# Kernel optimization log

Hardware: AMD Instinct MI355X
Metric: run time of the kernel (lower is better)

Reference implementation:

```python
import jax, jax.numpy as jnp
import numpy as np
from jax import lax

D_MODEL = 1024
STATE_DIM = 32
GROUPS = 8
GROUP_DIM = D_MODEL // GROUPS
DT_MIN = 0.001
DT_MAX = 0.1
EPS = 1e-6


def setup_inputs() -> dict:
    key = jax.random.key(0)
    ks = jax.random.split(key, 6)
    B, T = 4, 4096
    u = jax.random.normal(ks[0], (B, T, D_MODEL), dtype=jnp.float32)
    state = jnp.zeros((B, GROUPS, STATE_DIM), dtype=jnp.float32)
    A_log = jax.random.normal(ks[1], (GROUPS, STATE_DIM), dtype=jnp.float32) * 0.02
    B_param = jax.random.normal(ks[2], (GROUPS, STATE_DIM, GROUP_DIM), dtype=jnp.float32) * 0.02
    C = jax.random.normal(ks[3], (GROUPS, GROUP_DIM, STATE_DIM), dtype=jnp.float32) * 0.02
    Dp = jnp.zeros((GROUPS, GROUP_DIM), dtype=jnp.float32)
    dt_logit = jnp.zeros((GROUPS,), dtype=jnp.float32)
    return {"u": u, "state": state, "A_log": A_log, "B_param": B_param,
            "C": C, "Dp": Dp, "dt_logit": dt_logit}


def reference(u, state, A_log, B_param, C, Dp, dt_logit):
    Bsz, T, Dm = u.shape
    A = -jax.nn.softplus(A_log)                                  # [G,N]
    dt = DT_MIN + (DT_MAX - DT_MIN) * jax.nn.sigmoid(dt_logit)   # [G]
    dt_g = dt[:, None]                                           # [G,1]
    Abar = jnp.exp(A * dt_g)                                     # [G,N]
    # (exp(A dt) - 1)/A, stable for small |A|
    frac = jnp.where(jnp.abs(A) > EPS, (Abar - 1.0) / A,
                     jnp.broadcast_to(dt_g, A.shape))            # [G,N]
    Bbar = frac[..., None] * B_param                             # [G,N,gd]

    u_g = u.reshape(Bsz, T, GROUPS, GROUP_DIM)                   # [B,T,G,gd]
    # precompute input injections for all timesteps, then scan the LTI recurrence
    Bu = jnp.einsum('btgi,gni->btgn', u_g, Bbar)                 # [B,T,G,N]
    Bu_t = jnp.moveaxis(Bu, 1, 0)                                # [T,B,G,N]

    def step(s, bu):
        s = s * Abar + bu                                        # [B,G,N]
        return s, s

    s_final, states = lax.scan(step, state, Bu_t)                # states: [T,B,G,N]
    Cs = jnp.einsum('tbgn,gdn->btgd', states, C)                 # [B,T,G,gd]
    y = (Cs + Dp * u_g).reshape(Bsz, T, Dm)                      # [B,T,D]
    return y, s_final
```

## Files before the change

kernel.cpp:

```cpp
#include <hip/hip_runtime.h>
#include <hip/hip_bf16.h>

#define DM 1024
#define SD 32
#define NG 8
#define GD 128
#define BS 4
#define TT 4096
#define CL 64
#define NC (TT/CL)

typedef __attribute__((ext_vector_type(8))) short short8;
typedef __attribute__((ext_vector_type(4))) float f32x4;

#define WS_POWA  0
#define WS_STL   65536
#define WS_CARRY (WS_STL + 8388608)
#define WS_PAL   (WS_CARRY + 262144)

__device__ __forceinline__ unsigned short f2bf(float f) {
  __hip_bfloat16 h = __float2bfloat16(f);
  return __builtin_bit_cast(unsigned short, h);
}
__device__ __forceinline__ float bf2f(unsigned short h) {
  return __uint_as_float(((unsigned)h) << 16);
}
__device__ __forceinline__ float softplus_f(float x) {
  return (x > 20.f) ? x : log1pf(expf(x));
}
__device__ __forceinline__ short8 pack8(float4 a, float4 b) {
  short8 h;
  h[0]=(short)f2bf(a.x); h[1]=(short)f2bf(a.y); h[2]=(short)f2bf(a.z); h[3]=(short)f2bf(a.w);
  h[4]=(short)f2bf(b.x); h[5]=(short)f2bf(b.y); h[6]=(short)f2bf(b.z); h[7]=(short)f2bf(b.w);
  return h;
}

__global__ __launch_bounds__(64) void ka_bu_scan(const float* __restrict__ u,
                                                 const float* __restrict__ A_log,
                                                 const float* __restrict__ B_param,
                                                 const float* __restrict__ dt_logit,
                                                 unsigned char* __restrict__ ws) {
  const int bx = blockIdx.x;
  const int c = bx & (NC - 1);
  const int g = (bx >> 6) & (NG - 1);
  const int b = bx >> 9;
  const int l = threadIdx.x;
  const int lr = l & 15, lh = l >> 4;

  const float dtg = 0.001f + 0.099f * (1.f / (1.f + expf(-dt_logit[g])));

  float fracv[2];
  #pragma unroll
  for (int nt = 0; nt < 2; ++nt) {
    int n = nt * 16 + lr;
    float A = -softplus_f(A_log[g * SD + n]);
    float a = expf(A * dtg);
    fracv[nt] = (fabsf(A) > 1e-6f) ? (a - 1.f) / A : dtg;
  }
  float a_scan;
  {
    float A = -softplus_f(A_log[g * SD + (l & 31)]);
    a_scan = expf(A * dtg);
  }

  const float* bp = B_param + (size_t)g * SD * GD;
  short8 bfr[4][2];
  #pragma unroll
  for (int kt = 0; kt < 4; ++kt)
    #pragma unroll
    for (int nt = 0; nt < 2; ++nt) {
      const float* p = bp + (size_t)(nt * 16 + lr) * GD + kt * 32 + lh * 8;
      float4 v0 = *(const float4*)p;
      float4 v1 = *(const float4*)(p + 4);
      float s = fracv[nt];
      v0.x*=s; v0.y*=s; v0.z*=s; v0.w*=s;
      v1.x*=s; v1.y*=s; v1.z*=s; v1.w*=s;
      bfr[kt][nt] = pack8(v0, v1);
    }

  const float* up = u + ((size_t)b * TT + (size_t)c * CL) * DM + g * GD;
  float4 ub[2][4][2];
  #pragma unroll
  for (int kt = 0; kt < 2; ++kt)
    #pragma unroll
    for (int m = 0; m < 4; ++m) {
      const float* p = up + (size_t)(m * 16 + lr) * DM + kt * 32 + lh * 8;
      ub[kt][m][0] = *(const float4*)p;
      ub[kt][m][1] = *(const float4*)(p + 4);
    }

  f32x4 acc[4][2];
  #pragma unroll
  for (int m = 0; m < 4; ++m)
    #pragma unroll
    for (int nt = 0; nt < 2; ++nt)
      #pragma unroll
      for (int j = 0; j < 4; ++j) acc[m][nt][j] = 0.f;

  #pragma unroll
  for (int kt = 0; kt < 4; ++kt) {
    short8 af[4];
    #pragma unroll
    for (int m = 0; m < 4; ++m)
      af[m] = pack8(ub[kt & 1][m][0], ub[kt & 1][m][1]);
    if (kt < 2) {
      #pragma unroll
      for (int m = 0; m < 4; ++m) {
        const float* p = up + (size_t)(m * 16 + lr) * DM + (kt + 2) * 32 + lh * 8;
        ub[kt & 1][m][0] = *(const float4*)p;
        ub[kt & 1][m][1] = *(const float4*)(p + 4);
      }
    }
    #pragma unroll
    for (int m = 0; m < 4; ++m)
      #pragma unroll
      for (int nt = 0; nt < 2; ++nt)
        acc[m][nt] = __builtin_amdgcn_mfma_f32_16x16x32_bf16(af[m], bfr[kt][nt], acc[m][nt], 0, 0, 0);
  }

  __shared__ __align__(16) float sBu[CL * 33];
  __shared__ __align__(16) unsigned short sSt[CL * SD];
  #pragma unroll
  for (int m = 0; m < 4; ++m)
    #pragma unroll
    for (int nt = 0; nt < 2; ++nt)
      #pragma unroll
      for (int j = 0; j < 4; ++j) {
        int t = m * 16 + lh * 4 + j;
        sBu[t * 33 + (nt * 16 + lr)] = acc[m][nt][j];
      }
  __syncthreads();

  float* carry = (float*)(ws + WS_CARRY);
  if (l < SD) {
    float s = 0.f;
    #pragma unroll
    for (int t = 0; t < CL; ++t) {
      s = fmaf(s, a_scan, sBu[t * 33 + l]);
      sSt[t * SD + l] = f2bf(s);
    }
    carry[((b * NG + g) * NC + c) * SD + l] = s;
  }
  __syncthreads();

  unsigned short* stg = (unsigned short*)(ws + WS_STL) + ((size_t)((b * NC + c) * NG + g)) * CL * SD;
  #pragma unroll
  for (int p = 0; p < 4; ++p) {
    int off = (p * 64 + l) * 8;
    *(short8*)(stg + off) = *(short8*)(sSt + off);
  }

  if (b == 0 && c == 0 && l < SD) {
    float* powA = (float*)(ws + WS_POWA);
    float* powAL = (float*)(ws + WS_PAL);
    float p = 1.f;
    #pragma unroll
    for (int t = 0; t < CL; ++t) {
      p *= a_scan;
      powA[(g * CL + t) * SD + l] = p;
    }
    float aL = p;
    float q = 1.f;
    #pragma unroll
    for (int j = 0; j < CL; ++j) {
      powAL[(g * CL + j) * SD + l] = q;
      q *= aL;
    }
  }
}

__device__ __forceinline__ void kb_chunk(const unsigned short* __restrict__ stg,
                                         const float* __restrict__ powA,
                                         const float (&pr)[8],
                                         const short8 (&cf)[2],
                                         float* __restrict__ sY,
                                         const float* __restrict__ u,
                                         float* __restrict__ y,
                                         size_t rowbase,
                                         float4 dpv, bool need_u,
                                         int tid, int w, int lr, int lh) {
  short8 sf[4];
  #pragma unroll
  for (int tt = 0; tt < 4; ++tt) {
    int t = tt * 16 + lr;
    short8 sl = *(const short8*)(stg + t * SD + lh * 8);
    const float* pw = powA + t * SD + lh * 8;
    float4 pw0 = *(const float4*)pw;
    float4 pw1 = *(const float4*)(pw + 4);
    short8 hh;
    hh[0] = (short)f2bf(bf2f((unsigned short)sl[0]) + pw0.x * pr[0]);
    hh[1] = (short)f2bf(bf2f((unsigned short)sl[1]) + pw0.y * pr[1]);
    hh[2] = (short)f2bf(bf2f((unsigned short)sl[2]) + pw0.z * pr[2]);
    hh[3] = (short)f2bf(bf2f((unsigned short)sl[3]) + pw0.w * pr[3]);
    hh[4] = (short)f2bf(bf2f((unsigned short)sl[4]) + pw1.x * pr[4]);
    hh[5] = (short)f2bf(bf2f((unsigned short)sl[5]) + pw1.y * pr[5]);
    hh[6] = (short)f2bf(bf2f((unsigned short)sl[6]) + pw1.z * pr[6]);
    hh[7] = (short)f2bf(bf2f((unsigned short)sl[7]) + pw1.w * pr[7]);
    sf[tt] = hh;
  }

  f32x4 acc[2][4];
  #pragma unroll
  for (int dd = 0; dd < 2; ++dd)
    #pragma unroll
    for (int tt = 0; tt < 4; ++tt) {
      f32x4 z;
      #pragma unroll
      for (int j = 0; j < 4; ++j) z[j] = 0.f;
      acc[dd][tt] = __builtin_amdgcn_mfma_f32_16x16x32_bf16(cf[dd], sf[tt], z, 0, 0, 0);
    }

  const int sd4 = (tid & 31) * 4;
  #pragma unroll
  for (int tp = 0; tp < 2; ++tp) {
    __syncthreads();
    #pragma unroll
    for (int dd = 0; dd < 2; ++dd)
      #pragma unroll
      for (int q = 0; q < 2; ++q) {
        int tt = tp * 2 + q;
        int tl = q * 16 + lr;
        int d0 = (w * 2 + dd) * 16 + lh * 4;
        *(float4*)(sY + tl * 132 + d0) = (float4){acc[dd][tt][0], acc[dd][tt][1],
                                                  acc[dd][tt][2], acc[dd][tt][3]};
      }
    __syncthreads();
    #pragma unroll
    for (int r = 0; r < 4; ++r) {
      int tl = r * 8 + (tid >> 5);
      int t = tp * 32 + tl;
      float4 v = *(const float4*)(sY + tl * 132 + sd4);
      size_t off = rowbase + (size_t)t * DM + sd4;
      if (need_u) {
        float4 u4 = *(const float4*)(u + off);
        v.x += dpv.x * u4.x; v.y += dpv.y * u4.y;
        v.z += dpv.z * u4.z; v.w += dpv.w * u4.w;
      }
      *(float4*)(y + off) = v;
    }
  }
}

__global__ __launch_bounds__(256) void kb_y(const float* __restrict__ u,
                                            const float* __restrict__ state0,
                                            const float* __restrict__ C,
                                            const float* __restrict__ Dp,
                                            unsigned char* __restrict__ ws,
                                            float* __restrict__ y,
                                            float* __restrict__ sfin) {
  const int bx = blockIdx.x;
  const int pc = bx & (NC / 2 - 1);
  const int g = (bx >> 5) & (NG - 1);
  const int b = bx >> 8;
  const int c0 = pc * 2;
  const int tid = threadIdx.x;
  const int w = tid >> 6;
  const int l = tid & 63;
  const int lr = l & 15, lh = l >> 4;
  const int n = l & 31;

  const float* powA = (const float*)(ws + WS_POWA) + g * CL * SD;
  const float* powAL = (const float*)(ws + WS_PAL) + g * CL * SD;
  const float* carry = (const float*)(ws + WS_CARRY) + (size_t)(b * NG + g) * NC * SD;
  const unsigned short* stg0 = (const unsigned short*)(ws + WS_STL) + ((size_t)((b * NC + c0) * NG + g)) * CL * SD;
  const unsigned short* stg1 = stg0 + (size_t)NG * CL * SD;

  __shared__ __align__(16) float sY[32 * 132];

  bool need_u;
  {
    float2 dpc = *(const float2*)(Dp + g * GD + l * 2);
    need_u = __ballot((dpc.x != 0.f) || (dpc.y != 0.f)) != 0ULL;
  }

  float p0;
  {
    float a0 = 0.f, a1 = 0.f, a2 = 0.f, a3 = 0.f;
    int cc = 0;
    while (cc + 8 <= c0) {
      float ca[8], wt[8];
      #pragma unroll
      for (int e = 0; e < 8; ++e) {
        ca[e] = carry[(cc + e) * SD + n];
        wt[e] = powAL[(c0 - 1 - cc - e) * SD + n];
      }
      a0 = fmaf(wt[0], ca[0], a0); a1 = fmaf(wt[1], ca[1], a1);
      a2 = fmaf(wt[2], ca[2], a2); a3 = fmaf(wt[3], ca[3], a3);
      a0 = fmaf(wt[4], ca[4], a0); a1 = fmaf(wt[5], ca[5], a1);
      a2 = fmaf(wt[6], ca[6], a2); a3 = fmaf(wt[7], ca[7], a3);
      cc += 8;
    }
    for (; cc < c0; ++cc)
      a0 = fmaf(powAL[(c0 - 1 - cc) * SD + n], carry[cc * SD + n], a0);
    p0 = fmaf(state0[(b * NG + g) * SD + n], powAL[c0 * SD + n], (a0 + a1) + (a2 + a3));
  }
  const float aL = powA[(CL - 1) * SD + n];
  const float p1 = fmaf(p0, aL, carry[c0 * SD + n]);
  if (pc == NC / 2 - 1 && w == 0 && l < SD)
    sfin[(b * NG + g) * SD + l] = fmaf(p1, aL, carry[(NC - 1) * SD + l]);

  float pr0[8], pr1[8];
  #pragma unroll
  for (int e = 0; e < 8; ++e) {
    pr0[e] = __shfl(p0, lh * 8 + e);
    pr1[e] = __shfl(p1, lh * 8 + e);
  }

  const float* cp = C + (size_t)g * GD * SD;
  short8 cf[2];
  #pragma unroll
  for (int dd = 0; dd < 2; ++dd) {
    int d = (w * 2 + dd) * 16 + lr;
    const float* pp = cp + (size_t)d * SD + lh * 8;
    float4 v0 = *(const float4*)pp;
    float4 v1 = *(const float4*)(pp + 4);
    cf[dd] = pack8(v0, v1);
  }

  const int sd4 = (tid & 31) * 4;
  float4 dpv = *(const float4*)(Dp + g * GD + sd4);
  const size_t rowbase0 = ((size_t)b * TT + (size_t)c0 * CL) * DM + g * GD;

  kb_chunk(stg0, powA, pr0, cf, sY, u, y, rowbase0, dpv, need_u, tid, w, lr, lh);
  kb_chunk(stg1, powA, pr1, cf, sY, u, y, rowbase0 + (size_t)CL * DM, dpv, need_u, tid, w, lr, lh);
}

extern "C" void kernel_launch(void* const* d_in, const int* in_sizes, int n_in,
                              void* d_out, int out_size, void* d_ws, size_t ws_size,
                              hipStream_t stream) {
  const float* u       = (const float*)d_in[0];
  const float* state0  = (const float*)d_in[1];
  const float* A_log   = (const float*)d_in[2];
  const float* B_param = (const float*)d_in[3];
  const float* C       = (const float*)d_in[4];
  const float* Dp      = (const float*)d_in[5];
  const float* dtl     = (const float*)d_in[6];
  float* y = (float*)d_out;
  unsigned char* ws = (unsigned char*)d_ws;
  float* sfin = y + (size_t)BS * TT * DM;

  ka_bu_scan<<<dim3(BS * NG * NC), dim3(64), 0, stream>>>(u, A_log, B_param, dtl, ws);
  kb_y<<<dim3(BS * NG * NC / 2), dim3(256), 0, stream>>>(u, state0, C, Dp, ws, y, sfin);
}
```

Baseline: 43.87 us.

## Halve scan chunk length and process four chunks per output block

Reduces the per-chunk length from 64 to 32 timesteps, doubling the number of chunks and scan blocks, which shortens the serial in-chunk recurrence. The output kernel now processes four consecutive chunks per block, deriving each chunk's starting state by chaining carries, with the workspace layout and chunk-power table resized to match. This trades more blocks, more redundant B-fragment setup, and a longer inter-chunk carry prefix for a shorter sequential scan.

```diff
diff --git a/kernel.cpp b/kernel.cpp
--- a/kernel.cpp
+++ b/kernel.cpp
@@ -7,16 +7,17 @@
 #define GD 128
 #define BS 4
 #define TT 4096
-#define CL 64
+#define CL 32
 #define NC (TT/CL)
+#define SUBC 4
 
 typedef __attribute__((ext_vector_type(8))) short short8;
 typedef __attribute__((ext_vector_type(4))) float f32x4;
 
 #define WS_POWA  0
-#define WS_STL   65536
-#define WS_CARRY (WS_STL + 8388608)
-#define WS_PAL   (WS_CARRY + 262144)
+#define WS_PAL   32768
+#define WS_CARRY 163840
+#define WS_STL   688128
 
 __device__ __forceinline__ unsigned short f2bf(float f) {
   __hip_bfloat16 h = __float2bfloat16(f);
@@ -42,8 +43,8 @@
                                                  unsigned char* __restrict__ ws) {
   const int bx = blockIdx.x;
   const int c = bx & (NC - 1);
-  const int g = (bx >> 6) & (NG - 1);
-  const int b = bx >> 9;
+  const int g = (bx >> 7) & (NG - 1);
+  const int b = bx >> 10;
   const int l = threadIdx.x;
   const int lr = l & 15, lh = l >> 4;
 
@@ -79,19 +80,19 @@
     }
 
   const float* up = u + ((size_t)b * TT + (size_t)c * CL) * DM + g * GD;
-  float4 ub[2][4][2];
+  float4 ub[2][2][2];
   #pragma unroll
   for (int kt = 0; kt < 2; ++kt)
     #pragma unroll
-    for (int m = 0; m < 4; ++m) {
+    for (int m = 0; m < 2; ++m) {
       const float* p = up + (size_t)(m * 16 + lr) * DM + kt * 32 + lh * 8;
       ub[kt][m][0] = *(const float4*)p;
       ub[kt][m][1] = *(const float4*)(p + 4);
     }
 
-  f32x4 acc[4][2];
-  #pragma unroll
-  for (int m = 0; m < 4; ++m)
+  f32x4 acc[2][2];
+  #pragma unroll
+  for (int m = 0; m < 2; ++m)
     #pragma unroll
     for (int nt = 0; nt < 2; ++nt)
       #pragma unroll
@@ -99,20 +100,20 @@
 
   #pragma unroll
   for (int kt = 0; kt < 4; ++kt) {
-    short8 af[4];
-    #pragma unroll
-    for (int m = 0; m < 4; ++m)
+    short8 af[2];
+    #pragma unroll
+    for (int m = 0; m < 2; ++m)
       af[m] = pack8(ub[kt & 1][m][0], ub[kt & 1][m][1]);
     if (kt < 2) {
       #pragma unroll
-      for (int m = 0; m < 4; ++m) {
+      for (int m = 0; m < 2; ++m) {
         const float* p = up + (size_t)(m * 16 + lr) * DM + (kt + 2) * 32 + lh * 8;
         ub[kt & 1][m][0] = *(const float4*)p;
         ub[kt & 1][m][1] = *(const float4*)(p + 4);
       }
     }
     #pragma unroll
-    for (int m = 0; m < 4; ++m)
+    for (int m = 0; m < 2; ++m)
       #pragma unroll
       for (int nt = 0; nt < 2; ++nt)
         acc[m][nt] = __builtin_amdgcn_mfma_f32_16x16x32_bf16(af[m], bfr[kt][nt], acc[m][nt], 0, 0, 0);
@@ -121,7 +122,7 @@
   __shared__ __align__(16) float sBu[CL * 33];
   __shared__ __align__(16) unsigned short sSt[CL * SD];
   #pragma unroll
-  for (int m = 0; m < 4; ++m)
+  for (int m = 0; m < 2; ++m)
     #pragma unroll
     for (int nt = 0; nt < 2; ++nt)
       #pragma unroll
@@ -145,7 +146,7 @@
 
   unsigned short* stg = (unsigned short*)(ws + WS_STL) + ((size_t)((b * NC + c) * NG + g)) * CL * SD;
   #pragma unroll
-  for (int p = 0; p < 4; ++p) {
+  for (int p = 0; p < 2; ++p) {
     int off = (p * 64 + l) * 8;
     *(short8*)(stg + off) = *(short8*)(sSt + off);
   }
@@ -161,9 +162,8 @@
     }
     float aL = p;
     float q = 1.f;
-    #pragma unroll
-    for (int j = 0; j < CL; ++j) {
-      powAL[(g * CL + j) * SD + l] = q;
+    for (int j = 0; j < NC; ++j) {
+      powAL[(g * NC + j) * SD + l] = q;
       q *= aL;
     }
   }
@@ -171,7 +171,7 @@
 
 __device__ __forceinline__ void kb_chunk(const unsigned short* __restrict__ stg,
                                          const float* __restrict__ powA,
-                                         const float (&pr)[8],
+                                         float p,
                                          const short8 (&cf)[2],
                                          float* __restrict__ sY,
                                          const float* __restrict__ u,
@@ -179,9 +179,13 @@
                                          size_t rowbase,
                                          float4 dpv, bool need_u,
                                          int tid, int w, int lr, int lh) {
-  short8 sf[4];
-  #pragma unroll
-  for (int tt = 0; tt < 4; ++tt) {
+  float pr[8];
+  #pragma unroll
+  for (int e = 0; e < 8; ++e) pr[e] = __shfl(p, lh * 8 + e);
+
+  short8 sf[2];
+  #pragma unroll
+  for (int tt = 0; tt < 2; ++tt) {
     int t = tt * 16 + lr;
     short8 sl = *(const short8*)(stg + t * SD + lh * 8);
     const float* pw = powA + t * SD + lh * 8;
@@ -199,45 +203,40 @@
     sf[tt] = hh;
   }
 
-  f32x4 acc[2][4];
+  f32x4 acc[2][2];
   #pragma unroll
   for (int dd = 0; dd < 2; ++dd)
     #pragma unroll
-    for (int tt = 0; tt < 4; ++tt) {
+    for (int tt = 0; tt < 2; ++tt) {
       f32x4 z;
       #pragma unroll
       for (int j = 0; j < 4; ++j) z[j] = 0.f;
       acc[dd][tt] = __builtin_amdgcn_mfma_f32_16x16x32_bf16(cf[dd], sf[tt], z, 0, 0, 0);
     }
 
+  __syncthreads();
+  #pragma unroll
+  for (int dd = 0; dd < 2; ++dd)
+    #pragma unroll
+    for (int tt = 0; tt < 2; ++tt) {
+      int tl = tt * 16 + lr;
+      int d0 = (w * 2 + dd) * 16 + lh * 4;
+      *(float4*)(sY + tl * 132 + d0) = (float4){acc[dd][tt][0], acc[dd][tt][1],
+                                                acc[dd][tt][2], acc[dd][tt][3]};
+    }
+  __syncthreads();
   const int sd4 = (tid & 31) * 4;
   #pragma unroll
-  for (int tp = 0; tp < 2; ++tp) {
-    __syncthreads();
-    #pragma unroll
-    for (int dd = 0; dd < 2; ++dd)
-      #pragma unroll
-      for (int q = 0; q < 2; ++q) {
-        int tt = tp * 2 + q;
-        int tl = q * 16 + lr;
-        int d0 = (w * 2 + dd) * 16 + lh * 4;
-        *(float4*)(sY + tl * 132 + d0) = (float4){acc[dd][tt][0], acc[dd][tt][1],
-                                                  acc[dd][tt][2], acc[dd][tt][3]};
-      }
-    __syncthreads();
-    #pragma unroll
-    for (int r = 0; r < 4; ++r) {
-      int tl = r * 8 + (tid >> 5);
-      int t = tp * 32 + tl;
-      float4 v = *(const float4*)(sY + tl * 132 + sd4);
-      size_t off = rowbase + (size_t)t * DM + sd4;
-      if (need_u) {
-        float4 u4 = *(const float4*)(u + off);
-        v.x += dpv.x * u4.x; v.y += dpv.y * u4.y;
-        v.z += dpv.z * u4.z; v.w += dpv.w * u4.w;
-      }
-      *(float4*)(y + off) = v;
-    }
+  for (int r = 0; r < 4; ++r) {
+    int tl = r * 8 + (tid >> 5);
+    float4 v = *(const float4*)(sY + tl * 132 + sd4);
+    size_t off = rowbase + (size_t)tl * DM + sd4;
+    if (need_u) {
+      float4 u4 = *(const float4*)(u + off);
+      v.x += dpv.x * u4.x; v.y += dpv.y * u4.y;
+      v.z += dpv.z * u4.z; v.w += dpv.w * u4.w;
+    }
+    *(float4*)(y + off) = v;
   }
 }
 
@@ -249,10 +248,10 @@
                                             float* __restrict__ y,
                                             float* __restrict__ sfin) {
   const int bx = blockIdx.x;
-  const int pc = bx & (NC / 2 - 1);
+  const int pc = bx & (NC / SUBC - 1);
   const int g = (bx >> 5) & (NG - 1);
   const int b = bx >> 8;
-  const int c0 = pc * 2;
+  const int c0 = pc * SUBC;
   const int tid = threadIdx.x;
   const int w = tid >> 6;
   const int l = tid & 63;
@@ -260,10 +259,9 @@
   const int n = l & 31;
 
   const float* powA = (const float*)(ws + WS_POWA) + g * CL * SD;
-  const float* powAL = (const float*)(ws + WS_PAL) + g * CL * SD;
+  const float* powAL = (const float*)(ws + WS_PAL) + g * NC * SD;
   const float* carry = (const float*)(ws + WS_CARRY) + (size_t)(b * NG + g) * NC * SD;
-  const unsigned short* stg0 = (const unsigned short*)(ws + WS_STL) + ((size_t)((b * NC + c0) * NG + g)) * CL * SD;
-  const unsigned short* stg1 = stg0 + (size_t)NG * CL * SD;
+  const unsigned short* stbase = (const unsigned short*)(ws + WS_STL);
 
   __shared__ __align__(16) float sY[32 * 132];
 
@@ -295,16 +293,13 @@
     p0 = fmaf(state0[(b * NG + g) * SD + n], powAL[c0 * SD + n], (a0 + a1) + (a2 + a3));
   }
   const float aL = powA[(CL - 1) * SD + n];
-  const float p1 = fmaf(p0, aL, carry[c0 * SD + n]);
-  if (pc == NC / 2 - 1 && w == 0 && l < SD)
-    sfin[(b * NG + g) * SD + l] = fmaf(p1, aL, carry[(NC - 1) * SD + l]);
-
-  float pr0[8], pr1[8];
-  #pragma unroll
-  for (int e = 0; e < 8; ++e) {
-    pr0[e] = __shfl(p0, lh * 8 + e);
-    pr1[e] = __shfl(p1, lh * 8 + e);
-  }
+  float pch[SUBC];
+  pch[0] = p0;
+  #pragma unroll
+  for (int i = 1; i < SUBC; ++i)
+    pch[i] = fmaf(pch[i - 1], aL, carry[(c0 + i - 1) * SD + n]);
+  if (pc == NC / SUBC - 1 && w == 0 && l < SD)
+    sfin[(b * NG + g) * SD + l] = fmaf(pch[SUBC - 1], aL, carry[(NC - 1) * SD + l]);
 
   const float* cp = C + (size_t)g * GD * SD;
   short8 cf[2];
@@ -321,8 +316,12 @@
   float4 dpv = *(const float4*)(Dp + g * GD + sd4);
   const size_t rowbase0 = ((size_t)b * TT + (size_t)c0 * CL) * DM + g * GD;
 
-  kb_chunk(stg0, powA, pr0, cf, sY, u, y, rowbase0, dpv, need_u, tid, w, lr, lh);
-  kb_chunk(stg1, powA, pr1, cf, sY, u, y, rowbase0 + (size_t)CL * DM, dpv, need_u, tid, w, lr, lh);
+  #pragma unroll
+  for (int i = 0; i < SUBC; ++i) {
+    const unsigned short* stg = stbase + ((size_t)((b * NC + c0 + i) * NG + g)) * CL * SD;
+    kb_chunk(stg, powA, pch[i], cf, sY, u, y,
+             rowbase0 + (size_t)i * CL * DM, dpv, need_u, tid, w, lr, lh);
+  }
 }
 
 extern "C" void kernel_launch(void* const* d_in, const int* in_sizes, int n_in,
@@ -340,5 +339,5 @@
   float* sfin = y + (size_t)BS * TT * DM;
 
   ka_bu_scan<<<dim3(BS * NG * NC), dim3(64), 0, stream>>>(u, A_log, B_param, dtl, ws);
-  kb_y<<<dim3(BS * NG * NC / 2), dim3(256), 0, stream>>>(u, state0, C, Dp, ws, y, sfin);
-}
+  kb_y<<<dim3(BS * NG * NC / SUBC), dim3(256), 0, stream>>>(u, state0, C, Dp, ws, y, sfin);
+}
```

Result: slower. 48.39 us (+10.3%).
